# Kernel tuning notes

Hardware: AMD Instinct MI355X
Metric: run time of the kernel (lower is better)

The kernel has to match this reference:

```python
import math
import jax, jax.numpy as jnp
import numpy as np

D = 256       # d_model
R = 64        # low-rank bottleneck
E = 3         # num experts
KS = (1, 3, 5)
EPS = 0.1     # sinkhorn epsilon
ITERS = 10    # sinkhorn iterations


def _ln(x, g, b):
    m = jnp.mean(x, -1, keepdims=True)
    v = jnp.mean((x - m) ** 2, -1, keepdims=True)
    return (x - m) * jax.lax.rsqrt(v + 1e-5) * g + b


def _gelu(x):
    return jax.nn.gelu(x, approximate=False)  # torch nn.GELU default (erf)


def setup_inputs() -> dict:
    key = jax.random.key(0)
    ks = jax.random.split(key, 12)
    s = 0.02
    B, Lt, La = 16, 1024, 2048
    return {
        "text_feat": jax.random.normal(ks[0], (B, Lt, D), jnp.float32),
        "audio_feat": jax.random.normal(ks[1], (B, La, D), jnp.float32),
        # shared OT projection (LayerNorm + Linear, shared across modalities)
        "ln_g": jnp.ones((D,), jnp.float32),
        "ln_b": jnp.zeros((D,), jnp.float32),
        "W_sh": jax.random.normal(ks[2], (D, D), jnp.float32) * s,
        "b_sh": jnp.zeros((D,), jnp.float32),
        # contradiction router: Linear(d+1->d) GELU Linear(d->E)
        "Wr1": jax.random.normal(ks[3], (D, D + 1), jnp.float32) * s,
        "br1": jnp.zeros((D,), jnp.float32),
        "Wr2": jax.random.normal(ks[4], (E, D), jnp.float32) * s,
        "br2": jnp.zeros((E,), jnp.float32),
        # 3 low-rank conv experts (stacked where shapes match)
        "down_W": jax.random.normal(ks[5], (E, R, D), jnp.float32) * s,
        "down_b": jnp.zeros((E, R), jnp.float32),
        "conv_w1": jax.random.normal(ks[6], (R, R, 1), jnp.float32) * s,
        "conv_w3": jax.random.normal(ks[7], (R, R, 3), jnp.float32) * s,
        "conv_w5": jax.random.normal(ks[8], (R, R, 5), jnp.float32) * s,
        "conv_b": jnp.zeros((E, R), jnp.float32),
        "up_W": jax.random.normal(ks[9], (E, D, R), jnp.float32) * s,
        "up_b": jnp.zeros((E, D), jnp.float32),
        "en_g": jnp.ones((E, D), jnp.float32),
        "en_b": jnp.zeros((E, D), jnp.float32),
    }


def reference(text_feat, audio_feat, ln_g, ln_b, W_sh, b_sh, Wr1, br1, Wr2, br2,
              down_W, down_b, conv_w1, conv_w3, conv_w5, conv_b, up_W, up_b, en_g, en_b):
    B, Lt, _ = text_feat.shape
    La = audio_feat.shape[1]

    # ---- shared projection (dropout = identity at eval) ----
    Tp = _ln(text_feat, ln_g, ln_b) @ W_sh.T + b_sh      # [B,Lt,D]
    Ap = _ln(audio_feat, ln_g, ln_b) @ W_sh.T + b_sh     # [B,La,D]

    # ---- cosine cost ----
    Tn = Tp / jnp.maximum(jnp.linalg.norm(Tp, axis=-1, keepdims=True), 1e-12)
    An = Ap / jnp.maximum(jnp.linalg.norm(Ap, axis=-1, keepdims=True), 1e-12)
    cost = 1.0 - jnp.einsum('bmd,bnd->bmn', Tn, An)      # [B,Lt,La]

    # ---- log-domain Sinkhorn (uniform marginals, no masks) ----
    log_K = -cost / (EPS + 1e-8)
    log_mu = jnp.full((B, Lt), -math.log(Lt), jnp.float32)
    log_nu = jnp.full((B, La), -math.log(La), jnp.float32)
    lu = jnp.zeros((B, Lt), jnp.float32)
    lv = jnp.zeros((B, La), jnp.float32)
    for _ in range(ITERS):
        lu = log_mu - jax.scipy.special.logsumexp(log_K + lv[:, None, :], axis=-1)
        lu = jnp.nan_to_num(jnp.clip(lu, -1e9, 1e9), nan=0.0, posinf=1e9, neginf=-1e9)
        lv = log_nu - jax.scipy.special.logsumexp(log_K + lu[:, :, None], axis=1)
        lv = jnp.nan_to_num(jnp.clip(lv, -1e9, 1e9), nan=0.0, posinf=1e9, neginf=-1e9)
    pi = jnp.exp(lu[:, :, None] + log_K + lv[:, None, :])
    pi = jnp.nan_to_num(pi, nan=0.0, posinf=1.0, neginf=0.0)  # [B,Lt,La]

    A_al = jnp.einsum('bmn,bnd->bmd', pi, Ap)            # [B,Lt,D]
    S = jnp.sum(Tp * A_al, -1)                           # [B,Lt]
    resid = jnp.abs(Tp - A_al)                           # [B,Lt,D]

    # ---- contradiction router ----
    rin = jnp.concatenate([S[..., None], resid], -1)     # [B,Lt,D+1]
    G = jax.nn.softmax(_gelu(rin @ Wr1.T + br1) @ Wr2.T + br2, axis=-1)  # [B,Lt,E]

    # ---- multi-scale low-rank conv MoE over contradiction residual ----
    convs = (conv_w1, conv_w3, conv_w5)
    x = resid
    out = jnp.zeros_like(Tp)
    for e in range(E):
        h = _gelu(x @ down_W[e].T + down_b[e])           # [B,Lt,R]
        k = convs[e].shape[-1]
        pad = (k - 1) // 2
        hc = jax.lax.conv_general_dilated(
            h.transpose(0, 2, 1), convs[e], (1,), [(pad, pad)],
            dimension_numbers=('NCH', 'OIH', 'NCH')) + conv_b[e][None, :, None]
        h = _gelu(hc).transpose(0, 2, 1)                 # [B,Lt,R]
        h = h @ up_W[e].T + up_b[e]                      # [B,Lt,D]
        eo = _ln(h + x, en_g[e], en_b[e])
        out = out + G[..., e:e + 1] * eo
    return out
```

## Files before the change

kernel.cpp:

```cpp
#include <hip/hip_runtime.h>
#include <cstdio>

#define D_ 256
#define LT 1024
#define LA 2048
#define NB 16
#define RR_ 64
#define NRT (NB*LT)
#define NRA (NB*LA)

#define DECQ  (-0.080645161f)
#define DECQ2 (-0.11634637f)

typedef short bf16x8 __attribute__((ext_vector_type(8)));
typedef float f32x4 __attribute__((ext_vector_type(4)));

__device__ __forceinline__ float gelu_f(float x) {
    return 0.5f * x * (1.0f + erff(x * 0.70710678118654752f));
}
__device__ __forceinline__ unsigned short f2bf(float f) {
    union { float f; unsigned int i; } c; c.f = f;
    unsigned int x = c.i;
    return (unsigned short)((x + 0x7fffu + ((x >> 16) & 1u)) >> 16);
}
__device__ __forceinline__ float exp2_fast(float x) {
#if __has_builtin(__builtin_amdgcn_exp2f)
    return __builtin_amdgcn_exp2f(x);
#else
    float r; asm("v_exp_f32 %0, %1" : "=v"(r) : "v"(x)); return r;
#endif
}
__device__ __forceinline__ unsigned int cvt_pk_bf16(float lo, float hi) {
    unsigned int r;
    asm("v_cvt_pk_bf16_f32 %0, %1, %2" : "=v"(r) : "v"(lo), "v"(hi));
    return r;
}

__global__ __launch_bounds__(256) void k_prep_all(
    const float* __restrict__ W_sh, const float* __restrict__ down_W,
    const float* __restrict__ up_W, const float* __restrict__ Wr1,
    unsigned short* __restrict__ Wb, unsigned short* __restrict__ dWb,
    unsigned short* __restrict__ uWb, unsigned short* __restrict__ Wr1b)
{
    int i = blockIdx.x * 256 + threadIdx.x;
    if (i < 65536) Wb[i] = f2bf(W_sh[i]);
    else if (i < 114688) { int j = i - 65536; dWb[j] = f2bf(down_W[j]); }
    else if (i < 163840) { int j = i - 114688; uWb[j] = f2bf(up_W[j]); }
    else { int j = i - 163840; int n = j >> 8, k = j & 255; Wr1b[j] = f2bf(Wr1[(long)n * 257 + 1 + k]); }
}

__global__ __launch_bounds__(256) void k_lnproj_mfma(
    const float* __restrict__ X, const float* __restrict__ g, const float* __restrict__ bln,
    const unsigned short* __restrict__ Wb, const float* __restrict__ bsh,
    float* __restrict__ Pf, unsigned short* __restrict__ Nb)
{
    __shared__ short xb[64][264];
    __shared__ short Bs[256][40];
    int tid = threadIdx.x;
    long row0 = (long)blockIdx.x * 64;
    {
        int lane = tid & 31, rg = tid >> 5;
        float4 ga = *(const float4*)(g + lane * 8);
        float4 gb2 = *(const float4*)(g + lane * 8 + 4);
        float4 ba = *(const float4*)(bln + lane * 8);
        float4 bb2 = *(const float4*)(bln + lane * 8 + 4);
        for (int it = 0; it < 8; it++) {
            int r = it * 8 + rg;
            const float4* xp4 = (const float4*)(X + (row0 + r) * D_);
            float4 a = xp4[lane * 2], b = xp4[lane * 2 + 1];
            float s = a.x + a.y + a.z + a.w + b.x + b.y + b.z + b.w;
#pragma unroll
            for (int off = 16; off >= 1; off >>= 1) s += __shfl_xor(s, off);
            float mean = s * (1.0f / 256.0f);
            float q = (a.x - mean) * (a.x - mean) + (a.y - mean) * (a.y - mean)
                    + (a.z - mean) * (a.z - mean) + (a.w - mean) * (a.w - mean)
                    + (b.x - mean) * (b.x - mean) + (b.y - mean) * (b.y - mean)
                    + (b.z - mean) * (b.z - mean) + (b.w - mean) * (b.w - mean);
#pragma unroll
            for (int off = 16; off >= 1; off >>= 1) q += __shfl_xor(q, off);
            float ivar = rsqrtf(q * (1.0f / 256.0f) + 1e-5f);
            unsigned int u0 = f2bf((a.x - mean) * ivar * ga.x + ba.x);
            unsigned int u1 = f2bf((a.y - mean) * ivar * ga.y + ba.y);
            unsigned int u2 = f2bf((a.z - mean) * ivar * ga.z + ba.z);
            unsigned int u3 = f2bf((a.w - mean) * ivar * ga.w + ba.w);
            unsigned int u4 = f2bf((b.x - mean) * ivar * gb2.x + bb2.x);
            unsigned int u5 = f2bf((b.y - mean) * ivar * gb2.y + bb2.y);
            unsigned int u6 = f2bf((b.z - mean) * ivar * gb2.z + bb2.z);
            unsigned int u7 = f2bf((b.w - mean) * ivar * gb2.w + bb2.w);
            int4 pv;
            pv.x = (int)(u0 | (u1 << 16)); pv.y = (int)(u2 | (u3 << 16));
            pv.z = (int)(u4 | (u5 << 16)); pv.w = (int)(u6 | (u7 << 16));
            *(int4*)&xb[r][lane * 8] = pv;
        }
    }
    __syncthreads();
    int wid = tid >> 6, lane = tid & 63;
    int l15 = lane & 15, kq = lane >> 4;
    int m_local = wid * 16;
    f32x4 acc[16];
#pragma unroll
    for (int j = 0; j < 16; j++) acc[j] = (f32x4){0.f, 0.f, 0.f, 0.f};
    for (int kt = 0; kt < 8; kt++) {
        int k0 = kt * 32;
#pragma unroll
        for (int h = 0; h < 4; h++) {
            int idx = tid + 256 * h;
            int n = idx >> 2, qc = idx & 3;
            *(int4*)&Bs[n][qc * 8] = *(const int4*)(Wb + (long)n * D_ + k0 + qc * 8);
        }
        __syncthreads();
        bf16x8 af = *(const bf16x8*)&xb[m_local + l15][k0 + kq * 8];
#pragma unroll
        for (int j = 0; j < 16; j++) {
            bf16x8 bf = *(const bf16x8*)&Bs[j * 16 + l15][kq * 8];
            acc[j] = __builtin_amdgcn_mfma_f32_16x16x32_bf16(af, bf, acc[j], 0, 0, 0);
        }
        __syncthreads();
    }
#pragma unroll
    for (int j = 0; j < 16; j++) {
        float bv = bsh[j * 16 + l15];
#pragma unroll
        for (int r = 0; r < 4; r++) acc[j][r] += bv;
    }
    float sq[4] = {0.f, 0.f, 0.f, 0.f};
#pragma unroll
    for (int j = 0; j < 16; j++)
#pragma unroll
        for (int r = 0; r < 4; r++) sq[r] += acc[j][r] * acc[j][r];
#pragma unroll
    for (int off = 8; off >= 1; off >>= 1) {
#pragma unroll
        for (int r = 0; r < 4; r++) sq[r] += __shfl_xor(sq[r], off);
    }
    float rinv[4];
#pragma unroll
    for (int r = 0; r < 4; r++) rinv[r] = 1.0f / fmaxf(sqrtf(sq[r]), 1e-12f);
#pragma unroll
    for (int j = 0; j < 16; j++) {
        int col = j * 16 + l15;
#pragma unroll
        for (int r = 0; r < 4; r++) {
            long m = row0 + m_local + kq * 4 + r;
            if (Pf) Pf[m * D_ + col] = acc[j][r];
            Nb[m * D_ + col] = f2bf(acc[j][r] * rinv[r]);
        }
    }
}

__global__ __launch_bounds__(256) void k_transpose_bf(
    const unsigned short* __restrict__ Anb, unsigned short* __restrict__ ApbT)
{
    __shared__ short t[64][68];
    int b = blockIdx.x;
    int n0 = blockIdx.y * 64;
    int d0 = blockIdx.z * 64;
    int tid = threadIdx.x;
#pragma unroll
    for (int h = 0; h < 2; h++) {
        int c = tid + 256 * h;
        int nr = c >> 3, ch = c & 7;
        *(int4*)&t[nr][ch * 8] = *(const int4*)(Anb + ((long)b * LA + n0 + nr) * D_ + d0 + ch * 8);
    }
    __syncthreads();
#pragma unroll
    for (int h = 0; h < 2; h++) {
        int c = tid + 256 * h;
        int d = c >> 3, nch = c & 7;
        unsigned short v[8];
#pragma unroll
        for (int k = 0; k < 8; k++) v[k] = (unsigned short)t[nch * 8 + k][d];
        int4 ov;
        ov.x = (int)((unsigned int)v[0] | ((unsigned int)v[1] << 16));
        ov.y = (int)((unsigned int)v[2] | ((unsigned int)v[3] << 16));
        ov.z = (int)((unsigned int)v[4] | ((unsigned int)v[5] << 16));
        ov.w = (int)((unsigned int)v[6] | ((unsigned int)v[7] << 16));
        *(int4*)(ApbT + ((long)b * D_ + d0 + d) * LA + n0 + nch * 8) = ov;
    }
}

__global__ __launch_bounds__(256) void k_cost_mfma(
    const unsigned short* __restrict__ Tnb, const unsigned short* __restrict__ Anb,
    unsigned char* __restrict__ logK8, unsigned char* __restrict__ logK8T)
{
    __shared__ short sm[2][128][48];
    short (*As)[48] = sm[0];
    short (*Bs)[48] = sm[1];
    unsigned char* tile = (unsigned char*)sm;
    int b = blockIdx.x;
    int m_blk = blockIdx.y * 128, n_blk = blockIdx.z * 128;
    int tid = threadIdx.x;
    int wid = tid >> 6, lane = tid & 63;
    int l15 = lane & 15, kq = lane >> 4;
    int wm0 = (wid >> 1) * 64, wn0 = (wid & 1) * 64;
    const unsigned short* Ab = Tnb + ((long)b * LT + m_blk) * D_;
    const unsigned short* Bb = Anb + ((long)b * LA + n_blk) * D_;
    f32x4 acc[4][4];
#pragma unroll
    for (int i = 0; i < 4; i++)
#pragma unroll
        for (int j = 0; j < 4; j++) acc[i][j] = (f32x4){0.f, 0.f, 0.f, 0.f};
    for (int kt = 0; kt < 8; kt++) {
        int k0 = kt * 32;
#pragma unroll
        for (int h = 0; h < 2; h++) {
            int idx = tid + 256 * h;
            int row = idx >> 2, ch = idx & 3;
            *(int4*)&As[row][ch * 8] = *(const int4*)(Ab + (long)row * D_ + k0 + ch * 8);
            *(int4*)&Bs[row][ch * 8] = *(const int4*)(Bb + (long)row * D_ + k0 + ch * 8);
        }
        __syncthreads();
        bf16x8 af[4], bfv[4];
#pragma unroll
        for (int i = 0; i < 4; i++) af[i] = *(const bf16x8*)&As[wm0 + i * 16 + l15][kq * 8];
#pragma unroll
        for (int j = 0; j < 4; j++) bfv[j] = *(const bf16x8*)&Bs[wn0 + j * 16 + l15][kq * 8];
#pragma unroll
        for (int i = 0; i < 4; i++)
#pragma unroll
            for (int j = 0; j < 4; j++)
                acc[i][j] = __builtin_amdgcn_mfma_f32_16x16x32_bf16(af[i], bfv[j], acc[i][j], 0, 0, 0);
        __syncthreads();
    }
#pragma unroll
    for (int i = 0; i < 4; i++) {
#pragma unroll
        for (int j = 0; j < 4; j++) {
            int n = wn0 + j * 16 + l15;
            long base = ((long)b * LT + m_blk + wm0 + i * 16 + kq * 4) * (long)LA + n_blk + n;
            unsigned int pk = 0;
#pragma unroll
            for (int r = 0; r < 4; r++) {
                float q = rintf((1.0f - acc[i][j][r]) * 124.0f);
                q = fminf(fmaxf(q, 0.0f), 255.0f);
                unsigned int qb = (unsigned int)q;
                pk |= qb << (8 * r);
                logK8[base + (long)r * LA] = (unsigned char)qb;
            }
            *(unsigned int*)&tile[n * 144 + wm0 + i * 16 + kq * 4] = pk;
        }
    }
    __syncthreads();
#pragma unroll
    for (int h = 0; h < 4; h++) {
        int idx = tid + 256 * h;
        int row = idx >> 3, ch = idx & 7;
        int4 v = *(const int4*)&tile[row * 144 + ch * 16];
        *(int4*)(logK8T + ((long)b * LA + n_blk + row) * (long)LT + m_blk + ch * 16) = v;
    }
}

__global__ __launch_bounds__(256) void k_rowlse3(
    const unsigned char* __restrict__ logK8, const float* __restrict__ lv2,
    float* __restrict__ lu2, int first)
{
    __shared__ float red[2][2];
    int b = blockIdx.x & 15;
    int mseg = blockIdx.x >> 4;
    int tid = threadIdx.x;
    int row = tid >> 7;
    int ln = tid & 127;
    float lvv[16];
    if (!first) {
        const float* lvp = lv2 + (long)b * LA + ln * 16;
#pragma unroll
        for (int k = 0; k < 4; k++) {
            float4 l = *(const float4*)(lvp + k * 4);
            lvv[k * 4 + 0] = l.x; lvv[k * 4 + 1] = l.y;
            lvv[k * 4 + 2] = l.z; lvv[k * 4 + 3] = l.w;
        }
    } else {
#pragma unroll
        for (int k = 0; k < 16; k++) lvv[k] = 0.f;
    }
    const unsigned char* p = logK8 + ((long)b * LT + mseg * 2 + row) * (long)LA + ln * 16;
    uint4 w = *(const uint4*)p;
    unsigned int ws4[4] = {w.x, w.y, w.z, w.w};
    float s = 0.f;
#pragma unroll
    for (int k = 0; k < 4; k++) {
        unsigned int u = ws4[k];
        s += exp2_fast(fmaf((float)(u & 0xffu),         DECQ2, lvv[k * 4 + 0]));
        s += exp2_fast(fmaf((float)((u >> 8) & 0xffu),  DECQ2, lvv[k * 4 + 1]));
        s += exp2_fast(fmaf((float)((u >> 16) & 0xffu), DECQ2, lvv[k * 4 + 2]));
        s += exp2_fast(fmaf((float)(u >> 24),           DECQ2, lvv[k * 4 + 3]));
    }
#pragma unroll
    for (int off = 32; off >= 1; off >>= 1) s += __shfl_xor(s, off);
    if ((tid & 63) == 0) red[row][(tid >> 6) & 1] = s;
    __syncthreads();
    if (tid < 2) {
        float sr = red[tid][0] + red[tid][1];
        lu2[(long)b * LT + mseg * 2 + tid] = -10.0f - __log2f(sr);
    }
}

__global__ __launch_bounds__(256) void k_collse3(
    const unsigned char* __restrict__ logK8T, const float* __restrict__ lu2,
    float* __restrict__ lv2, int final_)
{
    int b = blockIdx.x & 15;
    int nseg = blockIdx.x >> 4;
    int tid = threadIdx.x;
    int wv = tid >> 6, lane = tid & 63;
    int c = nseg * 4 + wv;
    float lus[16];
    const float* lup = lu2 + (long)b * LT + lane * 16;
#pragma unroll
    for (int k = 0; k < 4; k++) {
        float4 l = *(const float4*)(lup + k * 4);
        lus[k * 4 + 0] = l.x; lus[k * 4 + 1] = l.y;
        lus[k * 4 + 2] = l.z; lus[k * 4 + 3] = l.w;
    }
    const unsigned char* p = logK8T + ((long)b * LA + c) * (long)LT + lane * 16;
    uint4 w = *(const uint4*)p;
    unsigned int ws4[4] = {w.x, w.y, w.z, w.w};
    float s = 0.f;
#pragma unroll
    for (int k = 0; k < 4; k++) {
        unsigned int u = ws4[k];
        s += exp2_fast(fmaf((float)(u & 0xffu),         DECQ2, lus[k * 4 + 0]));
        s += exp2_fast(fmaf((float)((u >> 8) & 0xffu),  DECQ2, lus[k * 4 + 1]));
        s += exp2_fast(fmaf((float)((u >> 16) & 0xffu), DECQ2, lus[k * 4 + 2]));
        s += exp2_fast(fmaf((float)(u >> 24),           DECQ2, lus[k * 4 + 3]));
    }
#pragma unroll
    for (int off = 32; off >= 1; off >>= 1) s += __shfl_xor(s, off);
    if (lane == 0) {
        lv2[(long)b * LA + c] = final_ ? (0.00048828125f / s)
                                       : (-11.0f - __log2f(s));
    }
}

__global__ __launch_bounds__(256) void k_scale_ev(
    unsigned short* __restrict__ ApbT, const float* __restrict__ ev)
{
    int b = blockIdx.x;
    int d = blockIdx.y;
    int tid = threadIdx.x;
    long off = ((long)b * D_ + d) * (long)LA + tid * 8;
    int4 v = *(const int4*)(ApbT + off);
    const float* ep = ev + (long)b * LA + tid * 8;
    float4 e0 = *(const float4*)ep, e1 = *(const float4*)(ep + 4);
    unsigned int u[4] = {(unsigned int)v.x, (unsigned int)v.y, (unsigned int)v.z, (unsigned int)v.w};
    float ee[8] = {e0.x, e0.y, e0.z, e0.w, e1.x, e1.y, e1.z, e1.w};
    unsigned int o[4];
#pragma unroll
    for (int k = 0; k < 4; k++) {
        float lo = __uint_as_float(u[k] << 16) * ee[2 * k];
        float hi = __uint_as_float(u[k] & 0xffff0000u) * ee[2 * k + 1];
        o[k] = cvt_pk_bf16(lo, hi);
    }
    int4 ov; ov.x = (int)o[0]; ov.y = (int)o[1]; ov.z = (int)o[2]; ov.w = (int)o[3];
    *(int4*)(ApbT + off) = ov;
}

__global__ __launch_bounds__(256) void k_pi2(
    const unsigned char* __restrict__ logK8, const unsigned short* __restrict__ Av,
    const float* __restrict__ lu2, float* __restrict__ Apart)
{
    __shared__ short As[64][56];
    __shared__ short Bs[256][56];
    __shared__ float eus[64];
    int b = blockIdx.x;
    int kh = blockIdx.y;
    int m_blk = blockIdx.z * 64;
    int nbase = kh * 1024;
    int tid = threadIdx.x;
    if (tid < 64) eus[tid] = exp2_fast(lu2[(long)b * LT + m_blk + tid]);
    int wid = tid >> 6, lane = tid & 63;
    int l15 = lane & 15, kq = lane >> 4;
    int wm0 = (wid & 1) * 32, wd0 = (wid >> 1) * 128;
    f32x4 acc[2][8];
#pragma unroll
    for (int i = 0; i < 2; i++)
#pragma unroll
        for (int j = 0; j < 8; j++) acc[i][j] = (f32x4){0.f, 0.f, 0.f, 0.f};
    const unsigned char* Kbase = logK8 + ((long)b * LT + m_blk) * (long)LA + nbase;
    const unsigned short* Bbase = Av + (long)b * D_ * (long)LA + nbase;
    int arow = tid >> 2, ac8 = (tid & 3) * 8;
    for (int kt = 0; kt < 32; kt++) {
        int n0 = kt * 32;
        {
            uint2 raw = *(const uint2*)(Kbase + (long)arow * LA + n0 + ac8);
            unsigned int w0 = raw.x, w1 = raw.y;
            float e0 = exp2_fast((float)(w0 & 0xffu) * DECQ2);
            float e1 = exp2_fast((float)((w0 >> 8) & 0xffu) * DECQ2);
            float e2 = exp2_fast((float)((w0 >> 16) & 0xffu) * DECQ2);
            float e3 = exp2_fast((float)(w0 >> 24) * DECQ2);
            float e4 = exp2_fast((float)(w1 & 0xffu) * DECQ2);
            float e5 = exp2_fast((float)((w1 >> 8) & 0xffu) * DECQ2);
            float e6 = exp2_fast((float)((w1 >> 16) & 0xffu) * DECQ2);
            float e7 = exp2_fast((float)(w1 >> 24) * DECQ2);
            int4 ov;
            ov.x = (int)cvt_pk_bf16(e0, e1); ov.y = (int)cvt_pk_bf16(e2, e3);
            ov.z = (int)cvt_pk_bf16(e4, e5); ov.w = (int)cvt_pk_bf16(e6, e7);
            *(int4*)&As[arow][ac8] = ov;
        }
#pragma unroll
        for (int h = 0; h < 4; h++) {
            int idx = tid + 256 * h;
            int row = idx >> 2, ch = idx & 3;
            *(int4*)&Bs[row][ch * 8] = *(const int4*)(Bbase + (long)row * LA + n0 + ch * 8);
        }
        __syncthreads();
        bf16x8 af[2], bfv[8];
        af[0] = *(const bf16x8*)&As[wm0 + l15][kq * 8];
        af[1] = *(const bf16x8*)&As[wm0 + 16 + l15][kq * 8];
#pragma unroll
        for (int j = 0; j < 8; j++) bfv[j] = *(const bf16x8*)&Bs[wd0 + j * 16 + l15][kq * 8];
#pragma unroll
        for (int i = 0; i < 2; i++)
#pragma unroll
            for (int j = 0; j < 8; j++)
                acc[i][j] = __builtin_amdgcn_mfma_f32_16x16x32_bf16(af[i], bfv[j], acc[i][j], 0, 0, 0);
        __syncthreads();
    }
    float* dst = Apart + (long)kh * (NB * (long)LT * D_);
#pragma unroll
    for (int i = 0; i < 2; i++) {
#pragma unroll
        for (int r = 0; r < 4; r++) {
            int rloc = wm0 + i * 16 + kq * 4 + r;
            float eu = eus[rloc];
            int m = m_blk + rloc;
            long obase = ((long)b * LT + m) * D_;
#pragma unroll
            for (int j = 0; j < 8; j++)
                dst[obase + wd0 + j * 16 + l15] = acc[i][j][r] * eu;
        }
    }
}

__global__ __launch_bounds__(256) void k_sresid(
    const float* __restrict__ Tp, const float* __restrict__ Apart,
    float* __restrict__ resid, unsigned short* __restrict__ residb, float* __restrict__ S)
{
    __shared__ float red[4];
    int b = blockIdx.x & 15;
    int m = blockIdx.x >> 4;
    long row = (long)b * LT + m;
    int tid = threadIdx.x;
    long idx = row * D_ + tid;
    float t = Tp[idx];
    float a = Apart[idx] + Apart[idx + (long)NB * LT * D_];
    float rr = fabsf(t - a);
    resid[idx] = rr;
    residb[idx] = f2bf(rr);
    float p = t * a;
#pragma unroll
    for (int off = 32; off >= 1; off >>= 1) p += __shfl_xor(p, off);
    if ((tid & 63) == 0) red[tid >> 6] = p;
    __syncthreads();
    if (tid == 0) S[row] = red[0] + red[1] + red[2] + red[3];
}

__global__ __launch_bounds__(256) void k_router_fused(
    const unsigned short* __restrict__ residb, const unsigned short* __restrict__ Wr1b,
    const float* __restrict__ Wr1, const float* __restrict__ br1,
    const float* __restrict__ S, const float* __restrict__ Wr2,
    const float* __restrict__ br2, float* __restrict__ G)
{
    __shared__ short xb[16][264];
    __shared__ short Bs[256][40];
    __shared__ float red[4][3][16];
    int tid = threadIdx.x;
    long row0 = (long)blockIdx.x * 16;
#pragma unroll
    for (int h = 0; h < 2; h++) {
        int idx = tid + 256 * h;
        int row = idx >> 5, ch = idx & 31;
        *(int4*)&xb[row][ch * 8] = *(const int4*)(residb + (row0 + row) * D_ + ch * 8);
    }
    __syncthreads();
    int wid = tid >> 6, lane = tid & 63;
    int l15 = lane & 15, kq = lane >> 4;
    f32x4 acc[4];
#pragma unroll
    for (int j = 0; j < 4; j++) acc[j] = (f32x4){0.f, 0.f, 0.f, 0.f};
    for (int kt = 0; kt < 8; kt++) {
        int k0 = kt * 32;
#pragma unroll
        for (int h = 0; h < 4; h++) {
            int idx = tid + 256 * h;
            int n = idx >> 2, qc = idx & 3;
            *(int4*)&Bs[n][qc * 8] = *(const int4*)(Wr1b + (long)n * D_ + k0 + qc * 8);
        }
        __syncthreads();
        bf16x8 af = *(const bf16x8*)&xb[l15][k0 + kq * 8];
#pragma unroll
        for (int j = 0; j < 4; j++) {
            bf16x8 bf = *(const bf16x8*)&Bs[wid * 64 + j * 16 + l15][kq * 8];
            acc[j] = __builtin_amdgcn_mfma_f32_16x16x32_bf16(af, bf, acc[j], 0, 0, 0);
        }
        __syncthreads();
    }
    float sv[4];
#pragma unroll
    for (int r = 0; r < 4; r++) sv[r] = S[row0 + kq * 4 + r];
    float le[3][4] = {};
#pragma unroll
    for (int j = 0; j < 4; j++) {
        int col = wid * 64 + j * 16 + l15;
        float w0 = Wr1[(long)col * 257];
        float bv = br1[col];
        float w2a = Wr2[col], w2b = Wr2[256 + col], w2c = Wr2[512 + col];
#pragma unroll
        for (int r = 0; r < 4; r++) {
            float hv = gelu_f(acc[j][r] + sv[r] * w0 + bv);
            le[0][r] += hv * w2a;
            le[1][r] += hv * w2b;
            le[2][r] += hv * w2c;
        }
    }
#pragma unroll
    for (int off = 8; off >= 1; off >>= 1)
#pragma unroll
        for (int e = 0; e < 3; e++)
#pragma unroll
            for (int r = 0; r < 4; r++) le[e][r] += __shfl_xor(le[e][r], off);
    if (l15 == 0) {
#pragma unroll
        for (int e = 0; e < 3; e++)
#pragma unroll
            for (int r = 0; r < 4; r++) red[wid][e][kq * 4 + r] = le[e][r];
    }
    __syncthreads();
    if (tid < 16) {
        float L0 = red[0][0][tid] + red[1][0][tid] + red[2][0][tid] + red[3][0][tid] + br2[0];
        float L1 = red[0][1][tid] + red[1][1][tid] + red[2][1][tid] + red[3][1][tid] + br2[1];
        float L2 = red[0][2][tid] + red[1][2][tid] + red[2][2][tid] + red[3][2][tid] + br2[2];
        float mx = fmaxf(L0, fmaxf(L1, L2));
        float e0 = __expf(L0 - mx), e1 = __expf(L1 - mx), e2 = __expf(L2 - mx);
        float inv = 1.0f / (e0 + e1 + e2);
        long m = row0 + tid;
        G[m] = e0 * inv; G[NRT + m] = e1 * inv; G[2 * NRT + m] = e2 * inv;
    }
}

__global__ __launch_bounds__(256) void k_down_mfma(
    const unsigned short* __restrict__ residb, const unsigned short* __restrict__ dWb,
    const float* __restrict__ db, float* __restrict__ hall)
{
    __shared__ short xb[64][264];
    __shared__ short Bs[64][40];
    int tid = threadIdx.x;
    int e = blockIdx.y;
    int b = blockIdx.x & 15;
    int mseg = blockIdx.x >> 4;
    long row0 = (long)b * LT + mseg * 64;
    const unsigned short* dWe = dWb + (long)e * RR_ * D_;
    float* h = hall + (long)e * NRT * RR_;
#pragma unroll
    for (int hh = 0; hh < 8; hh++) {
        int idx = tid + 256 * hh;
        int row = idx >> 5, ch = idx & 31;
        *(int4*)&xb[row][ch * 8] = *(const int4*)(residb + (row0 + row) * D_ + ch * 8);
    }
    __syncthreads();
    int wid = tid >> 6, lane = tid & 63;
    int l15 = lane & 15, kq = lane >> 4;
    int m_local = wid * 16;
    f32x4 acc[4];
#pragma unroll
    for (int j = 0; j < 4; j++) acc[j] = (f32x4){0.f, 0.f, 0.f, 0.f};
    for (int kt = 0; kt < 8; kt++) {
        int k0 = kt * 32;
        {
            int n = tid >> 2, qc = tid & 3;
            *(int4*)&Bs[n][qc * 8] = *(const int4*)(dWe + (long)n * D_ + k0 + qc * 8);
        }
        __syncthreads();
        bf16x8 af = *(const bf16x8*)&xb[m_local + l15][k0 + kq * 8];
#pragma unroll
        for (int j = 0; j < 4; j++) {
            bf16x8 bf = *(const bf16x8*)&Bs[j * 16 + l15][kq * 8];
            acc[j] = __builtin_amdgcn_mfma_f32_16x16x32_bf16(af, bf, acc[j], 0, 0, 0);
        }
        __syncthreads();
    }
#pragma unroll
    for (int j = 0; j < 4; j++) {
        int col = j * 16 + l15;
        float bv = db[e * RR_ + col];
#pragma unroll
        for (int r = 0; r < 4; r++) {
            long m = row0 + m_local + kq * 4 + r;
            h[m * RR_ + col] = gelu_f(acc[j][r] + bv);
        }
    }
}

__global__ __launch_bounds__(256) void k_conv_all(
    const float* __restrict__ hall, const float* __restrict__ cw1,
    const float* __restrict__ cw3, const float* __restrict__ cw5,
    const float* __restrict__ conv_b, unsigned short* __restrict__ hcbb)
{
    __shared__ float hs[68][68];
    __shared__ float wt[64][64];
    int e = blockIdx.y;
    const float* w = (e == 0) ? cw1 : ((e == 1) ? cw3 : cw5);
    int ksz = (e == 0) ? 1 : ((e == 1) ? 3 : 5);
    const float* h = hall + (long)e * NRT * RR_;
    unsigned short* hcb = hcbb + (long)e * NRT * RR_;
    const float* cb = conv_b + e * 64;
    int b = blockIdx.x & 15;
    int m0 = (blockIdx.x >> 4) * 64;
    int tid = threadIdx.x;
    int pad = (ksz - 1) >> 1;
    for (int idx = tid; idx < 68 * 16; idx += 256) {
        int mr = idx >> 4, i4 = idx & 15;
        int mm = m0 - 2 + mr;
        float4 vv = { 0.f, 0.f, 0.f, 0.f };
        if (mm >= 0 && mm < LT) vv = *(const float4*)(h + ((long)b * LT + mm) * RR_ + i4 * 4);
        *(float4*)&hs[mr][i4 * 4] = vv;
    }
    int tx = tid & 15, ty = tid >> 4;
    float acc[4][4] = {};
    for (int t = 0; t < ksz; t++) {
        __syncthreads();
        for (int idx = tid; idx < 4096; idx += 256) {
            int i = idx & 63, j = idx >> 6;
            wt[i][j] = w[(long)j * RR_ * ksz + i * ksz + t];
        }
        __syncthreads();
        int roff = ty * 4 + 2 + t - pad;
        for (int i4 = 0; i4 < 16; i4++) {
            float4 h0 = *(const float4*)&hs[roff + 0][i4 * 4];
            float4 h1 = *(const float4*)&hs[roff + 1][i4 * 4];
            float4 h2 = *(const float4*)&hs[roff + 2][i4 * 4];
            float4 h3 = *(const float4*)&hs[roff + 3][i4 * 4];
            float hh[4][4] = { { h0.x, h0.y, h0.z, h0.w }, { h1.x, h1.y, h1.z, h1.w },
                               { h2.x, h2.y, h2.z, h2.w }, { h3.x, h3.y, h3.z, h3.w } };
#pragma unroll
            for (int s = 0; s < 4; s++) {
                float4 wv = *(const float4*)&wt[i4 * 4 + s][tx * 4];
#pragma unroll
                for (int r = 0; r < 4; r++) {
                    acc[r][0] += hh[r][s] * wv.x;
                    acc[r][1] += hh[r][s] * wv.y;
                    acc[r][2] += hh[r][s] * wv.z;
                    acc[r][3] += hh[r][s] * wv.w;
                }
            }
        }
    }
    float4 bb = *(const float4*)(cb + tx * 4);
#pragma unroll
    for (int r = 0; r < 4; r++) {
        long m = (long)b * LT + m0 + ty * 4 + r;
        unsigned long long pv =
              (unsigned long long)f2bf(gelu_f(acc[r][0] + bb.x))
            | ((unsigned long long)f2bf(gelu_f(acc[r][1] + bb.y)) << 16)
            | ((unsigned long long)f2bf(gelu_f(acc[r][2] + bb.z)) << 32)
            | ((unsigned long long)f2bf(gelu_f(acc[r][3] + bb.w)) << 48);
        *(unsigned long long*)(hcb + m * RR_ + tx * 4) = pv;
    }
}

__global__ __launch_bounds__(256) void k_up3(
    const unsigned short* __restrict__ hcbb, const unsigned short* __restrict__ uWb,
    const float* __restrict__ up_b, const float* __restrict__ resid,
    const float* __restrict__ en_g, const float* __restrict__ en_b,
    const float* __restrict__ G, float* __restrict__ out)
{
    __shared__ short hs[64][88];
    __shared__ short Bs[256][40];
    int tid = threadIdx.x;
    int b = blockIdx.x & 15;
    int mseg = blockIdx.x >> 4;
    long row0 = (long)b * LT + mseg * 64;
    int wid = tid >> 6, lane = tid & 63;
    int l15 = lane & 15, kq = lane >> 4;
    int m_local = wid * 16;
    long mrow[4];
#pragma unroll
    for (int r = 0; r < 4; r++) mrow[r] = row0 + m_local + kq * 4 + r;
    f32x4 outacc[16];
#pragma unroll
    for (int j = 0; j < 16; j++) outacc[j] = (f32x4){0.f, 0.f, 0.f, 0.f};
    for (int e = 0; e < 3; e++) {
        __syncthreads();
        const unsigned short* hcb = hcbb + (long)e * NRT * RR_;
        const unsigned short* uWe = uWb + (long)e * 16384;
#pragma unroll
        for (int hh = 0; hh < 2; hh++) {
            int idx = tid + 256 * hh;
            int row = idx >> 3, ch = idx & 7;
            *(int4*)&hs[row][ch * 8] = *(const int4*)(hcb + (row0 + row) * RR_ + ch * 8);
        }
        f32x4 acc[16];
#pragma unroll
        for (int j = 0; j < 16; j++) acc[j] = (f32x4){0.f, 0.f, 0.f, 0.f};
        for (int kt = 0; kt < 2; kt++) {
            int k0 = kt * 32;
#pragma unroll
            for (int hh = 0; hh < 4; hh++) {
                int idx = tid + 256 * hh;
                int n = idx >> 2, qc = idx & 3;
                *(int4*)&Bs[n][qc * 8] = *(const int4*)(uWe + (long)n * RR_ + k0 + qc * 8);
            }
            __syncthreads();
            bf16x8 af = *(const bf16x8*)&hs[m_local + l15][k0 + kq * 8];
#pragma unroll
            for (int j = 0; j < 16; j++) {
                bf16x8 bf = *(const bf16x8*)&Bs[j * 16 + l15][kq * 8];
                acc[j] = __builtin_amdgcn_mfma_f32_16x16x32_bf16(af, bf, acc[j], 0, 0, 0);
            }
            __syncthreads();
        }
        const float* ub = up_b + e * 256;
#pragma unroll
        for (int j = 0; j < 16; j++) {
            int col = j * 16 + l15;
            float bv = ub[col];
#pragma unroll
            for (int r = 0; r < 4; r++)
                acc[j][r] += bv + resid[mrow[r] * D_ + col];
        }
        float s[4] = {0.f, 0.f, 0.f, 0.f};
#pragma unroll
        for (int j = 0; j < 16; j++)
#pragma unroll
            for (int r = 0; r < 4; r++) s[r] += acc[j][r];
#pragma unroll
        for (int off = 8; off >= 1; off >>= 1)
#pragma unroll
            for (int r = 0; r < 4; r++) s[r] += __shfl_xor(s[r], off);
        float mn[4];
#pragma unroll
        for (int r = 0; r < 4; r++) mn[r] = s[r] * (1.0f / 256.0f);
        float q[4] = {0.f, 0.f, 0.f, 0.f};
#pragma unroll
        for (int j = 0; j < 16; j++)
#pragma unroll
            for (int r = 0; r < 4; r++) { float d = acc[j][r] - mn[r]; q[r] += d * d; }
#pragma unroll
        for (int off = 8; off >= 1; off >>= 1)
#pragma unroll
            for (int r = 0; r < 4; r++) q[r] += __shfl_xor(q[r], off);
        float iv[4], gv[4];
#pragma unroll
        for (int r = 0; r < 4; r++) {
            iv[r] = rsqrtf(q[r] * (1.0f / 256.0f) + 1e-5f);
            gv[r] = G[(long)e * NRT + mrow[r]];
        }
        const float* eg = en_g + e * 256;
        const float* eb = en_b + e * 256;
#pragma unroll
        for (int j = 0; j < 16; j++) {
            int col = j * 16 + l15;
            float egc = eg[col], ebc = eb[col];
#pragma unroll
            for (int r = 0; r < 4; r++)
                outacc[j][r] += gv[r] * ((acc[j][r] - mn[r]) * iv[r] * egc + ebc);
        }
    }
#pragma unroll
    for (int j = 0; j < 16; j++) {
        int col = j * 16 + l15;
#pragma unroll
        for (int r = 0; r < 4; r++)
            out[mrow[r] * D_ + col] = outacc[j][r];
    }
}

extern "C" void kernel_launch(void* const* d_in, const int* in_sizes, int n_in,
                              void* d_out, int out_size, void* d_ws, size_t ws_size,
                              hipStream_t stream)
{
    const float* text   = (const float*)d_in[0];
    const float* audio  = (const float*)d_in[1];
    const float* ln_g   = (const float*)d_in[2];
    const float* ln_b   = (const float*)d_in[3];
    const float* W_sh   = (const float*)d_in[4];
    const float* b_sh   = (const float*)d_in[5];
    const float* Wr1    = (const float*)d_in[6];
    const float* br1    = (const float*)d_in[7];
    const float* Wr2    = (const float*)d_in[8];
    const float* br2    = (const float*)d_in[9];
    const float* down_W = (const float*)d_in[10];
    const float* down_b = (const float*)d_in[11];
    const float* cw1    = (const float*)d_in[12];
    const float* cw3    = (const float*)d_in[13];
    const float* cw5    = (const float*)d_in[14];
    const float* conv_b = (const float*)d_in[15];
    const float* up_W   = (const float*)d_in[16];
    const float* up_b   = (const float*)d_in[17];
    const float* en_g   = (const float*)d_in[18];
    const float* en_b   = (const float*)d_in[19];

    float* ws = (float*)d_ws;
    float*          Tp    = ws;
    unsigned short* Tnb   = (unsigned short*)(ws + 4194304);
    unsigned short* Anb   = (unsigned short*)(ws + 6291456);
    unsigned short* ApbT  = (unsigned short*)(ws + 10485760);
    unsigned char*  logK8 = (unsigned char*)(ws + 14680064);
    float*          Apart = ws + 23068672;
    float*          resid = ws + 31457280;
    unsigned short* residb= (unsigned short*)(ws + 35651584);
    float*          lu2   = ws + 37748736;
    float*          lv2   = ws + 37765120;
    float*          Sb    = ws + 37797888;
    float*          Gb    = ws + 37814272;
    unsigned short* Wb    = (unsigned short*)(ws + 37863424);
    unsigned short* dWb   = (unsigned short*)(ws + 37896192);
    unsigned short* uWb   = (unsigned short*)(ws + 37920768);
    unsigned short* Wr1b  = (unsigned short*)(ws + 37945344);
    size_t need_bytes = (size_t)37978112 * 4;
    if (ws_size < need_bytes) {
        fprintf(stderr, "kernel_launch: ws_size %zu < needed %zu\n", ws_size, need_bytes);
        return;
    }
    float*          hall = ws + 14680064;
    unsigned short* hcbb = (unsigned short*)(ws + 17825792);
    unsigned char*  logK8T = (unsigned char*)(ws + 23068672);

    k_prep_all<<<896, 256, 0, stream>>>(W_sh, down_W, up_W, Wr1, Wb, dWb, uWb, Wr1b);
    k_lnproj_mfma<<<NRT / 64, 256, 0, stream>>>(text, ln_g, ln_b, Wb, b_sh, Tp, Tnb);
    k_lnproj_mfma<<<NRA / 64, 256, 0, stream>>>(audio, ln_g, ln_b, Wb, b_sh, nullptr, Anb);
    k_transpose_bf<<<dim3(NB, LA / 64, D_ / 64), 256, 0, stream>>>(Anb, ApbT);
    k_cost_mfma<<<dim3(NB, LT / 128, LA / 128), 256, 0, stream>>>(Tnb, Anb, logK8, logK8T);
    for (int it = 0; it < 10; it++) {
        k_rowlse3<<<NRT / 2, 256, 0, stream>>>(logK8, lv2, lu2, it == 0 ? 1 : 0);
        k_collse3<<<NB * (LA / 4), 256, 0, stream>>>(logK8T, lu2, lv2, it == 9 ? 1 : 0);
    }
    k_scale_ev<<<dim3(NB, D_), 256, 0, stream>>>(ApbT, lv2);
    k_pi2<<<dim3(NB, 2, LT / 64), 256, 0, stream>>>(logK8, ApbT, lu2, Apart);
    k_sresid<<<NRT, 256, 0, stream>>>(Tp, Apart, resid, residb, Sb);
    k_router_fused<<<NRT / 16, 256, 0, stream>>>(residb, Wr1b, Wr1, br1, Sb, Wr2, br2, Gb);
    k_down_mfma<<<dim3(NRT / 64, 3), 256, 0, stream>>>(residb, dWb, down_b, hall);
    k_conv_all<<<dim3(NRT / 64, 3), 256, 0, stream>>>(hall, cw1, cw3, cw5, conv_b, hcbb);
    k_up3<<<NRT / 64, 256, 0, stream>>>(hcbb, uWb, up_b, resid, en_g, en_b, Gb, (float*)d_out);
}
```

Before: 534.2 us.

## Fuse text/audio projection with transpose and fold column scaling into pi kernel

Merges the two LayerNorm+projection launches and the separate bf16 transpose into a single kernel; audio blocks write the transposed ApbT tile from shared memory directly. The final-iteration column scaling pass (k_scale_ev) is removed, and the column potential lv2 is instead added inside the exponent in k_pi2, which loads it into shared memory. This removes launches and full passes over ApbT at the cost of extra LDS traffic and an extra FMA per element, and it changes the rounding order of the transport-plan weights. Several scalar bf16 packs are also replaced with the packed conversion instruction.

```diff
diff --git a/kernel.cpp b/kernel.cpp
--- a/kernel.cpp
+++ b/kernel.cpp
@@ -49,15 +49,22 @@
     else { int j = i - 163840; int n = j >> 8, k = j & 255; Wr1b[j] = f2bf(Wr1[(long)n * 257 + 1 + k]); }
 }
 
-__global__ __launch_bounds__(256) void k_lnproj_mfma(
-    const float* __restrict__ X, const float* __restrict__ g, const float* __restrict__ bln,
+__global__ __launch_bounds__(256) void k_lnproj_fused(
+    const float* __restrict__ Xt, const float* __restrict__ Xa,
+    const float* __restrict__ g, const float* __restrict__ bln,
     const unsigned short* __restrict__ Wb, const float* __restrict__ bsh,
-    float* __restrict__ Pf, unsigned short* __restrict__ Nb)
-{
-    __shared__ short xb[64][264];
-    __shared__ short Bs[256][40];
-    int tid = threadIdx.x;
-    long row0 = (long)blockIdx.x * 64;
+    float* __restrict__ Tp, unsigned short* __restrict__ Tnb,
+    unsigned short* __restrict__ Anb, unsigned short* __restrict__ ApbT)
+{
+    __shared__ short smem[64 * 264 + 256 * 40];
+    short (*xb)[264] = (short(*)[264])smem;
+    short (*Bs)[40]  = (short(*)[40])(smem + 64 * 264);
+    short (*tt)[72]  = (short(*)[72])smem;
+    int tid = threadIdx.x;
+    int bid = blockIdx.x;
+    bool is_text = bid < (NRT / 64);
+    const float* X = is_text ? Xt : Xa;
+    long row0 = is_text ? (long)bid * 64 : (long)(bid - NRT / 64) * 64;
     {
         int lane = tid & 31, rg = tid >> 5;
         float4 ga = *(const float4*)(g + lane * 8);
@@ -79,17 +86,17 @@
 #pragma unroll
             for (int off = 16; off >= 1; off >>= 1) q += __shfl_xor(q, off);
             float ivar = rsqrtf(q * (1.0f / 256.0f) + 1e-5f);
-            unsigned int u0 = f2bf((a.x - mean) * ivar * ga.x + ba.x);
-            unsigned int u1 = f2bf((a.y - mean) * ivar * ga.y + ba.y);
-            unsigned int u2 = f2bf((a.z - mean) * ivar * ga.z + ba.z);
-            unsigned int u3 = f2bf((a.w - mean) * ivar * ga.w + ba.w);
-            unsigned int u4 = f2bf((b.x - mean) * ivar * gb2.x + bb2.x);
-            unsigned int u5 = f2bf((b.y - mean) * ivar * gb2.y + bb2.y);
-            unsigned int u6 = f2bf((b.z - mean) * ivar * gb2.z + bb2.z);
-            unsigned int u7 = f2bf((b.w - mean) * ivar * gb2.w + bb2.w);
+            float v0 = (a.x - mean) * ivar * ga.x + ba.x;
+            float v1 = (a.y - mean) * ivar * ga.y + ba.y;
+            float v2 = (a.z - mean) * ivar * ga.z + ba.z;
+            float v3 = (a.w - mean) * ivar * ga.w + ba.w;
+            float v4 = (b.x - mean) * ivar * gb2.x + bb2.x;
+            float v5 = (b.y - mean) * ivar * gb2.y + bb2.y;
+            float v6 = (b.z - mean) * ivar * gb2.z + bb2.z;
+            float v7 = (b.w - mean) * ivar * gb2.w + bb2.w;
             int4 pv;
-            pv.x = (int)(u0 | (u1 << 16)); pv.y = (int)(u2 | (u3 << 16));
-            pv.z = (int)(u4 | (u5 << 16)); pv.w = (int)(u6 | (u7 << 16));
+            pv.x = (int)cvt_pk_bf16(v0, v1); pv.y = (int)cvt_pk_bf16(v2, v3);
+            pv.z = (int)cvt_pk_bf16(v4, v5); pv.w = (int)cvt_pk_bf16(v6, v7);
             *(int4*)&xb[r][lane * 8] = pv;
         }
     }
@@ -136,46 +143,39 @@
     float rinv[4];
 #pragma unroll
     for (int r = 0; r < 4; r++) rinv[r] = 1.0f / fmaxf(sqrtf(sq[r]), 1e-12f);
-#pragma unroll
-    for (int j = 0; j < 16; j++) {
-        int col = j * 16 + l15;
-#pragma unroll
-        for (int r = 0; r < 4; r++) {
-            long m = row0 + m_local + kq * 4 + r;
-            if (Pf) Pf[m * D_ + col] = acc[j][r];
-            Nb[m * D_ + col] = f2bf(acc[j][r] * rinv[r]);
-        }
-    }
-}
-
-__global__ __launch_bounds__(256) void k_transpose_bf(
-    const unsigned short* __restrict__ Anb, unsigned short* __restrict__ ApbT)
-{
-    __shared__ short t[64][68];
-    int b = blockIdx.x;
-    int n0 = blockIdx.y * 64;
-    int d0 = blockIdx.z * 64;
-    int tid = threadIdx.x;
-#pragma unroll
-    for (int h = 0; h < 2; h++) {
-        int c = tid + 256 * h;
-        int nr = c >> 3, ch = c & 7;
-        *(int4*)&t[nr][ch * 8] = *(const int4*)(Anb + ((long)b * LA + n0 + nr) * D_ + d0 + ch * 8);
-    }
-    __syncthreads();
-#pragma unroll
-    for (int h = 0; h < 2; h++) {
-        int c = tid + 256 * h;
-        int d = c >> 3, nch = c & 7;
-        unsigned short v[8];
-#pragma unroll
-        for (int k = 0; k < 8; k++) v[k] = (unsigned short)t[nch * 8 + k][d];
-        int4 ov;
-        ov.x = (int)((unsigned int)v[0] | ((unsigned int)v[1] << 16));
-        ov.y = (int)((unsigned int)v[2] | ((unsigned int)v[3] << 16));
-        ov.z = (int)((unsigned int)v[4] | ((unsigned int)v[5] << 16));
-        ov.w = (int)((unsigned int)v[6] | ((unsigned int)v[7] << 16));
-        *(int4*)(ApbT + ((long)b * D_ + d0 + d) * LA + n0 + nch * 8) = ov;
+    if (is_text) {
+#pragma unroll
+        for (int j = 0; j < 16; j++) {
+            int col = j * 16 + l15;
+#pragma unroll
+            for (int r = 0; r < 4; r++) {
+                long m = row0 + m_local + kq * 4 + r;
+                Tp[m * D_ + col] = acc[j][r];
+                Tnb[m * D_ + col] = f2bf(acc[j][r] * rinv[r]);
+            }
+        }
+    } else {
+#pragma unroll
+        for (int j = 0; j < 16; j++) {
+            int col = j * 16 + l15;
+#pragma unroll
+            for (int r = 0; r < 4; r++) {
+                int rloc = m_local + kq * 4 + r;
+                unsigned short qv = f2bf(acc[j][r] * rinv[r]);
+                Anb[(row0 + rloc) * D_ + col] = qv;
+                tt[col][rloc] = (short)qv;
+            }
+        }
+        __syncthreads();
+        int b = (int)(row0 >> 11);
+        int n0 = (int)(row0 & 2047);
+#pragma unroll
+        for (int h = 0; h < 8; h++) {
+            int ci = tid + 256 * h;
+            int col = ci >> 3, nch = ci & 7;
+            int4 v = *(const int4*)&tt[col][nch * 8];
+            *(int4*)(ApbT + ((long)b * D_ + col) * LA + n0 + nch * 8) = v;
+        }
     }
 }
 
@@ -297,7 +297,7 @@
 
 __global__ __launch_bounds__(256) void k_collse3(
     const unsigned char* __restrict__ logK8T, const float* __restrict__ lu2,
-    float* __restrict__ lv2, int final_)
+    float* __restrict__ lv2)
 {
     int b = blockIdx.x & 15;
     int nseg = blockIdx.x >> 4;
@@ -326,48 +326,26 @@
     }
 #pragma unroll
     for (int off = 32; off >= 1; off >>= 1) s += __shfl_xor(s, off);
-    if (lane == 0) {
-        lv2[(long)b * LA + c] = final_ ? (0.00048828125f / s)
-                                       : (-11.0f - __log2f(s));
-    }
-}
-
-__global__ __launch_bounds__(256) void k_scale_ev(
-    unsigned short* __restrict__ ApbT, const float* __restrict__ ev)
-{
-    int b = blockIdx.x;
-    int d = blockIdx.y;
-    int tid = threadIdx.x;
-    long off = ((long)b * D_ + d) * (long)LA + tid * 8;
-    int4 v = *(const int4*)(ApbT + off);
-    const float* ep = ev + (long)b * LA + tid * 8;
-    float4 e0 = *(const float4*)ep, e1 = *(const float4*)(ep + 4);
-    unsigned int u[4] = {(unsigned int)v.x, (unsigned int)v.y, (unsigned int)v.z, (unsigned int)v.w};
-    float ee[8] = {e0.x, e0.y, e0.z, e0.w, e1.x, e1.y, e1.z, e1.w};
-    unsigned int o[4];
-#pragma unroll
-    for (int k = 0; k < 4; k++) {
-        float lo = __uint_as_float(u[k] << 16) * ee[2 * k];
-        float hi = __uint_as_float(u[k] & 0xffff0000u) * ee[2 * k + 1];
-        o[k] = cvt_pk_bf16(lo, hi);
-    }
-    int4 ov; ov.x = (int)o[0]; ov.y = (int)o[1]; ov.z = (int)o[2]; ov.w = (int)o[3];
-    *(int4*)(ApbT + off) = ov;
+    if (lane == 0) lv2[(long)b * LA + c] = -11.0f - __log2f(s);
 }
 
 __global__ __launch_bounds__(256) void k_pi2(
-    const unsigned char* __restrict__ logK8, const unsigned short* __restrict__ Av,
-    const float* __restrict__ lu2, float* __restrict__ Apart)
+    const unsigned char* __restrict__ logK8, const unsigned short* __restrict__ Ap,
+    const float* __restrict__ lu2, const float* __restrict__ lv2,
+    float* __restrict__ Apart)
 {
     __shared__ short As[64][56];
     __shared__ short Bs[256][56];
+    __shared__ float lv_s[1024];
     __shared__ float eus[64];
     int b = blockIdx.x;
     int kh = blockIdx.y;
     int m_blk = blockIdx.z * 64;
     int nbase = kh * 1024;
     int tid = threadIdx.x;
+    for (int i = tid; i < 1024; i += 256) lv_s[i] = lv2[(long)b * LA + nbase + i];
     if (tid < 64) eus[tid] = exp2_fast(lu2[(long)b * LT + m_blk + tid]);
+    __syncthreads();
     int wid = tid >> 6, lane = tid & 63;
     int l15 = lane & 15, kq = lane >> 4;
     int wm0 = (wid & 1) * 32, wd0 = (wid >> 1) * 128;
@@ -377,21 +355,22 @@
 #pragma unroll
         for (int j = 0; j < 8; j++) acc[i][j] = (f32x4){0.f, 0.f, 0.f, 0.f};
     const unsigned char* Kbase = logK8 + ((long)b * LT + m_blk) * (long)LA + nbase;
-    const unsigned short* Bbase = Av + (long)b * D_ * (long)LA + nbase;
+    const unsigned short* Bbase = Ap + (long)b * D_ * (long)LA + nbase;
     int arow = tid >> 2, ac8 = (tid & 3) * 8;
     for (int kt = 0; kt < 32; kt++) {
         int n0 = kt * 32;
         {
             uint2 raw = *(const uint2*)(Kbase + (long)arow * LA + n0 + ac8);
+            const float* lvp = &lv_s[n0 + ac8];
             unsigned int w0 = raw.x, w1 = raw.y;
-            float e0 = exp2_fast((float)(w0 & 0xffu) * DECQ2);
-            float e1 = exp2_fast((float)((w0 >> 8) & 0xffu) * DECQ2);
-            float e2 = exp2_fast((float)((w0 >> 16) & 0xffu) * DECQ2);
-            float e3 = exp2_fast((float)(w0 >> 24) * DECQ2);
-            float e4 = exp2_fast((float)(w1 & 0xffu) * DECQ2);
-            float e5 = exp2_fast((float)((w1 >> 8) & 0xffu) * DECQ2);
-            float e6 = exp2_fast((float)((w1 >> 16) & 0xffu) * DECQ2);
-            float e7 = exp2_fast((float)(w1 >> 24) * DECQ2);
+            float e0 = exp2_fast(fmaf((float)(w0 & 0xffu),         DECQ2, lvp[0]));
+            float e1 = exp2_fast(fmaf((float)((w0 >> 8) & 0xffu),  DECQ2, lvp[1]));
+            float e2 = exp2_fast(fmaf((float)((w0 >> 16) & 0xffu), DECQ2, lvp[2]));
+            float e3 = exp2_fast(fmaf((float)(w0 >> 24),           DECQ2, lvp[3]));
+            float e4 = exp2_fast(fmaf((float)(w1 & 0xffu),         DECQ2, lvp[4]));
+            float e5 = exp2_fast(fmaf((float)((w1 >> 8) & 0xffu),  DECQ2, lvp[5]));
+            float e6 = exp2_fast(fmaf((float)((w1 >> 16) & 0xffu), DECQ2, lvp[6]));
+            float e7 = exp2_fast(fmaf((float)(w1 >> 24),           DECQ2, lvp[7]));
             int4 ov;
             ov.x = (int)cvt_pk_bf16(e0, e1); ov.y = (int)cvt_pk_bf16(e2, e3);
             ov.z = (int)cvt_pk_bf16(e4, e5); ov.w = (int)cvt_pk_bf16(e6, e7);
@@ -650,10 +629,8 @@
     for (int r = 0; r < 4; r++) {
         long m = (long)b * LT + m0 + ty * 4 + r;
         unsigned long long pv =
-              (unsigned long long)f2bf(gelu_f(acc[r][0] + bb.x))
-            | ((unsigned long long)f2bf(gelu_f(acc[r][1] + bb.y)) << 16)
-            | ((unsigned long long)f2bf(gelu_f(acc[r][2] + bb.z)) << 32)
-            | ((unsigned long long)f2bf(gelu_f(acc[r][3] + bb.w)) << 48);
+              (unsigned long long)cvt_pk_bf16(gelu_f(acc[r][0] + bb.x), gelu_f(acc[r][1] + bb.y))
+            | ((unsigned long long)cvt_pk_bf16(gelu_f(acc[r][2] + bb.z), gelu_f(acc[r][3] + bb.w)) << 32);
         *(unsigned long long*)(hcb + m * RR_ + tx * 4) = pv;
     }
 }
@@ -817,16 +794,14 @@
     unsigned char*  logK8T = (unsigned char*)(ws + 23068672);
 
     k_prep_all<<<896, 256, 0, stream>>>(W_sh, down_W, up_W, Wr1, Wb, dWb, uWb, Wr1b);
-    k_lnproj_mfma<<<NRT / 64, 256, 0, stream>>>(text, ln_g, ln_b, Wb, b_sh, Tp, Tnb);
-    k_lnproj_mfma<<<NRA / 64, 256, 0, stream>>>(audio, ln_g, ln_b, Wb, b_sh, nullptr, Anb);
-    k_transpose_bf<<<dim3(NB, LA / 64, D_ / 64), 256, 0, stream>>>(Anb, ApbT);
+    k_lnproj_fused<<<(NRT + NRA) / 64, 256, 0, stream>>>(text, audio, ln_g, ln_b, Wb, b_sh,
+                                                         Tp, Tnb, Anb, ApbT);
     k_cost_mfma<<<dim3(NB, LT / 128, LA / 128), 256, 0, stream>>>(Tnb, Anb, logK8, logK8T);
     for (int it = 0; it < 10; it++) {
         k_rowlse3<<<NRT / 2, 256, 0, stream>>>(logK8, lv2, lu2, it == 0 ? 1 : 0);
-        k_collse3<<<NB * (LA / 4), 256, 0, stream>>>(logK8T, lu2, lv2, it == 9 ? 1 : 0);
-    }
-    k_scale_ev<<<dim3(NB, D_), 256, 0, stream>>>(ApbT, lv2);
-    k_pi2<<<dim3(NB, 2, LT / 64), 256, 0, stream>>>(logK8, ApbT, lu2, Apart);
+        k_collse3<<<NB * (LA / 4), 256, 0, stream>>>(logK8T, lu2, lv2);
+    }
+    k_pi2<<<dim3(NB, 2, LT / 64), 256, 0, stream>>>(logK8, ApbT, lu2, lv2, Apart);
     k_sresid<<<NRT, 256, 0, stream>>>(Tp, Apart, resid, residb, Sb);
     k_router_fused<<<NRT / 16, 256, 0, stream>>>(residb, Wr1b, Wr1, br1, Sb, Wr2, br2, Gb);
     k_down_mfma<<<dim3(NRT / 64, 3), 256, 0, stream>>>(residb, dWb, down_b, hall);
```

Measured after the change: 532.1 us. About the same (-0.4%).
